# Kernel tuning notes

Hardware: AMD Instinct MI355X
Metric: run time of the kernel (lower is better)

The kernel has to match this reference:

```python
import jax, jax.numpy as jnp
import numpy as np

# norse LIFRefracParameters defaults
TAU_SYN_INV = 200.0
TAU_MEM_INV = 100.0
V_LEAK = 0.0
V_TH = 1.0
V_RESET = 0.0
ALPHA = 100.0       # SuperSpike surrogate slope
RHO_RESET = 5.0     # refractory period (steps)
DT = 0.001


@jax.custom_vjp
def superspike(x):
    # Heaviside forward, SuperSpike surrogate backward
    return (x > 0).astype(x.dtype)

def _ss_fwd(x):
    return superspike(x), x

def _ss_bwd(x, g):
    return (g / (ALPHA * jnp.abs(x) + 1.0) ** 2,)

superspike.defvjp(_ss_fwd, _ss_bwd)


def lif_mc_refrac_step(inp, z, v, i, rho, input_weights, recurrent_weights, g_coupling):
    # --- lif_mc_step ---
    dv = DT * TAU_MEM_INV * ((V_LEAK - v) + i)
    v_decayed = v + dv + v @ g_coupling.T          # [B,H] compartment coupling GEMM
    i_decayed = i - DT * TAU_SYN_INV * i
    z_new = superspike(v_decayed - V_TH)
    v_new = (1.0 - z_new) * v_decayed + z_new * V_RESET
    i_new = i_decayed + inp @ input_weights.T + z @ recurrent_weights.T  # two GEMMs
    # --- refractory update ---
    refrac_mask = superspike(rho)
    v_new = (1.0 - refrac_mask) * v_new + refrac_mask * v  # hold v while refractory
    z_new = (1.0 - refrac_mask) * z_new                    # suppress spikes
    rho_new = (1.0 - z_new) * jnp.maximum(rho - refrac_mask, 0.0) + z_new * RHO_RESET
    return z_new, v_new, i_new, rho_new


def setup_inputs() -> dict:
    key = jax.random.key(0)
    ks = jax.random.split(key, 8)
    B, I, H = 4096, 2048, 2048
    inp = jax.random.normal(ks[0], (B, I), jnp.float32)
    z = jax.random.uniform(ks[1], (B, H), jnp.float32)
    v = jax.random.normal(ks[2], (B, H), jnp.float32)
    i = jax.random.normal(ks[3], (B, H), jnp.float32)
    rho = jax.random.normal(ks[4], (B, H), jnp.float32)  # ~half neurons refractory
    input_weights = jax.random.normal(ks[5], (H, I), jnp.float32) / np.sqrt(I).astype(np.float32)
    recurrent_weights = jax.random.normal(ks[6], (H, H), jnp.float32) / np.sqrt(H).astype(np.float32)
    g_coupling = jax.random.normal(ks[7], (H, H), jnp.float32) / np.sqrt(H).astype(np.float32)
    return dict(inp=inp, z=z, v=v, i=i, rho=rho,
                input_weights=input_weights,
                recurrent_weights=recurrent_weights,
                g_coupling=g_coupling)


def reference(inp, z, v, i, rho, input_weights, recurrent_weights, g_coupling):
    return lif_mc_refrac_step(inp, z, v, i, rho, input_weights, recurrent_weights, g_coupling)
```

## Files before the change

kernel.cpp:

```cpp
#include <hip/hip_runtime.h>


#define HDIM 2048
#define BATCH 4096
#define KIN 2048
#define BM 128
#define BN 128
#define BK 32
#define MARGIN 0.02f
#define FLAG_LDS_CAP 1024

typedef _Float16 f16x8 __attribute__((ext_vector_type(8)));
typedef __fp16 h16x2 __attribute__((ext_vector_type(2)));
typedef float f32x4 __attribute__((ext_vector_type(4)));

template <typename T>
__device__ __forceinline__ void stage(const T* src, int ldk, int row0, int k0,
                                      T* lds_tile, int t) {
  constexpr int CHN = (BK * (int)sizeof(T)) / 16;
  constexpr int EPC = 16 / (int)sizeof(T);
#pragma unroll
  for (int j = 0; j < (BM * CHN) / 256; ++j) {
    const int u = j * 256 + t;
    const int r = u / CHN;
    const int cs = u & (CHN - 1);
    const int c = cs ^ (((r * CHN) >> 3) & (CHN - 1));
    const T* g = src + (size_t)(row0 + r) * ldk + k0 + c * EPC;
    __builtin_amdgcn_global_load_lds(
        (const __attribute__((address_space(1))) void*)(T*)g,
        (__attribute__((address_space(3))) void*)(lds_tile + u * EPC), 16, 0, 0);
  }
}

__device__ __forceinline__ f16x8 read_frag(const _Float16* tile, int r, int q) {
  const int slot = r * 4 + (q ^ ((r >> 1) & 3));
  return *(const f16x8*)(tile + slot * 8);
}
__device__ __forceinline__ f16x8 read_frag(const float* tile, int r, int q) {
  const int s = r & 7;
  const f32x4 a = *(const f32x4*)(tile + (r * 8 + ((2 * q) ^ s)) * 4);
  const f32x4 b = *(const f32x4*)(tile + (r * 8 + ((2 * q + 1) ^ s)) * 4);
  f16x8 o;
  h16x2 p;
  p = __builtin_amdgcn_cvt_pkrtz(a[0], a[1]); o[0] = (_Float16)p[0]; o[1] = (_Float16)p[1];
  p = __builtin_amdgcn_cvt_pkrtz(a[2], a[3]); o[2] = (_Float16)p[0]; o[3] = (_Float16)p[1];
  p = __builtin_amdgcn_cvt_pkrtz(b[0], b[1]); o[4] = (_Float16)p[0]; o[5] = (_Float16)p[1];
  p = __builtin_amdgcn_cvt_pkrtz(b[2], b[3]); o[6] = (_Float16)p[0]; o[7] = (_Float16)p[1];
  return o;
}

template <typename T>
__global__ __launch_bounds__(256, 4)
void k_gemm(const T* vA, const T* inpA, const T* zA,
            const T* gB, const T* WiB, const T* WrB,
            const float* v, const float* cur_in, const float* rho,
            float* z_out, float* v_out, float* rho_out, float* i_out,
            unsigned* flag_cnt, unsigned* flag_list, unsigned flag_cap) {
  __shared__ T As[2][BM * BK];
  __shared__ T Bs[2][BN * BK];
  __shared__ unsigned s_cnt;
  __shared__ unsigned s_base;
  __shared__ unsigned s_idx[FLAG_LDS_CAP];
  const int t = threadIdx.x;
  const int bid = blockIdx.x;
  const int x = bid & 7;
  const int j = bid >> 3;
  const int role = (j >> 5) & 1;
  const int jj = (j & 31) | ((j >> 6) << 5);
  const int mg = x & 3, ng = x >> 2;
  const int m0 = (mg * 8 + (jj >> 3)) * BM;
  const int n0 = (ng * 8 + (jj & 7)) * BN;

  const int wave = t >> 6, lane = t & 63;
  const int wm = (wave >> 1) * 64, wn = (wave & 1) * 64;
  const int lrow = lane & 15, quad = lane >> 4;

  const int kmax = role ? 2 * KIN : KIN;
  const int NT = kmax / BK;

  auto pick = [&](int k0, const T*& Ap, const T*& Bp) {
    if (role == 0)      { Ap = vA;   Bp = gB;  }
    else if (k0 < KIN)  { Ap = inpA; Bp = WiB; }
    else                { Ap = zA;   Bp = WrB; }
  };

  {
    const T *Ap, *Bp;
    pick(0, Ap, Bp);
    stage(Ap, KIN, m0, 0, As[0], t);
    stage(Bp, KIN, n0, 0, Bs[0], t);
  }
  if (t == 0) s_cnt = 0;

  f32x4 acc[4][4] = {};
#pragma unroll 2
  for (int it = 0; it < NT; ++it) {
    const int cur = it & 1;
    if (it + 1 < NT) {
      const int k0n = (it + 1) * BK;
      const T *Ap, *Bp;
      pick(k0n, Ap, Bp);
      const int kl = k0n & (KIN - 1);
      stage(Ap, KIN, m0, kl, As[cur ^ 1], t);
      stage(Bp, KIN, n0, kl, Bs[cur ^ 1], t);
      if constexpr (sizeof(T) == 2)
        asm volatile("s_waitcnt vmcnt(4)" ::: "memory");
      else
        asm volatile("s_waitcnt vmcnt(8)" ::: "memory");
    } else {
      asm volatile("s_waitcnt vmcnt(0)" ::: "memory");
    }
    __builtin_amdgcn_s_barrier();
    asm volatile("" ::: "memory");

    f16x8 af[4], bf[4];
#pragma unroll
    for (int mi = 0; mi < 4; ++mi) af[mi] = read_frag(As[cur], wm + mi * 16 + lrow, quad);
#pragma unroll
    for (int ni = 0; ni < 4; ++ni) bf[ni] = read_frag(Bs[cur], wn + ni * 16 + lrow, quad);
#pragma unroll
    for (int mi = 0; mi < 4; ++mi)
#pragma unroll
      for (int ni = 0; ni < 4; ++ni)
        acc[mi][ni] =
            __builtin_amdgcn_mfma_f32_16x16x32_f16(af[mi], bf[ni], acc[mi][ni], 0, 0, 0);

    asm volatile("" ::: "memory");
    __builtin_amdgcn_s_barrier();
  }

  if (role == 0) {
#pragma unroll
    for (int mi = 0; mi < 4; ++mi)
#pragma unroll
      for (int r = 0; r < 4; ++r) {
        const int row = m0 + wm + mi * 16 + quad * 4 + r;
#pragma unroll
        for (int ni = 0; ni < 4; ++ni) {
          const int col = n0 + wn + ni * 16 + lrow;
          const size_t idx = (size_t)row * HDIM + col;
          const float P = acc[mi][ni][r];
          const float vv = v[idx], ii = cur_in[idx], rr = rho[idx];
          const float vd = vv + 0.1f * (ii - vv) + P;
          float zo, vo, ro;
          if (rr > 0.0f) {
            zo = 0.0f; vo = vv; ro = fmaxf(rr - 1.0f, 0.0f);
          } else {
            const bool zs = vd > 1.0f;
            zo = zs ? 1.0f : 0.0f;
            vo = zs ? 0.0f : vd;
            ro = zs ? 5.0f : fmaxf(rr, 0.0f);
            if (fabsf(vd - 1.0f) < MARGIN) {
              unsigned p = atomicAdd(&s_cnt, 1u);
              if (p < FLAG_LDS_CAP) s_idx[p] = (unsigned)idx;
              else {
                unsigned q = atomicAdd(flag_cnt, 1u);
                if (q < flag_cap) flag_list[q] = (unsigned)idx;
              }
            }
          }
          z_out[idx] = zo; v_out[idx] = vo; rho_out[idx] = ro;
        }
      }
    __syncthreads();
    unsigned n = s_cnt;
    if (n > FLAG_LDS_CAP) n = FLAG_LDS_CAP;
    if (t == 0) s_base = atomicAdd(flag_cnt, n);
    __syncthreads();
    for (unsigned u = t; u < n; u += 256) {
      const unsigned d = s_base + u;
      if (d < flag_cap) flag_list[d] = s_idx[u];
    }
  } else {
#pragma unroll
    for (int mi = 0; mi < 4; ++mi)
#pragma unroll
      for (int r = 0; r < 4; ++r) {
        const int row = m0 + wm + mi * 16 + quad * 4 + r;
#pragma unroll
        for (int ni = 0; ni < 4; ++ni) {
          const int col = n0 + wn + ni * 16 + lrow;
          const size_t idx = (size_t)row * HDIM + col;
          const float ii = cur_in[idx];
          i_out[idx] = (ii - 0.2f * ii) + acc[mi][ni][r];
        }
      }
  }
}

__global__ void k_cast(const float* __restrict__ v, const float* __restrict__ inp,
                       const float* __restrict__ z, const float* __restrict__ g,
                       const float* __restrict__ Wi, const float* __restrict__ Wr,
                       _Float16* __restrict__ dst, unsigned* __restrict__ flag_cnt) {
  if (blockIdx.x == 0 && threadIdx.x == 0) *flag_cnt = 0;
  const size_t NA = (size_t)BATCH * HDIM, NB = (size_t)HDIM * HDIM;
  const size_t TOT = (3 * NA + 3 * NB) / 8;
  const size_t w = (size_t)blockIdx.x * blockDim.x + threadIdx.x;
  if (w >= TOT) return;
  const size_t e = w * 8;
  const float* s; size_t off;
  if      (e < NA)          { s = v;   off = e; }
  else if (e < 2 * NA)      { s = inp; off = e - NA; }
  else if (e < 3 * NA)      { s = z;   off = e - 2 * NA; }
  else if (e < 3 * NA + NB) { s = g;   off = e - 3 * NA; }
  else if (e < 3 * NA + 2 * NB) { s = Wi; off = e - 3 * NA - NB; }
  else                      { s = Wr;  off = e - 3 * NA - 2 * NB; }
  const f32x4 a = *(const f32x4*)(s + off);
  const f32x4 b = *(const f32x4*)(s + off + 4);
  f16x8 o; h16x2 p;
  p = __builtin_amdgcn_cvt_pkrtz(a[0], a[1]); o[0] = (_Float16)p[0]; o[1] = (_Float16)p[1];
  p = __builtin_amdgcn_cvt_pkrtz(a[2], a[3]); o[2] = (_Float16)p[0]; o[3] = (_Float16)p[1];
  p = __builtin_amdgcn_cvt_pkrtz(b[0], b[1]); o[4] = (_Float16)p[0]; o[5] = (_Float16)p[1];
  p = __builtin_amdgcn_cvt_pkrtz(b[2], b[3]); o[6] = (_Float16)p[0]; o[7] = (_Float16)p[1];
  *(f16x8*)(dst + e) = o;
}

__global__ void k_zero_cnt(unsigned* p) { if (threadIdx.x == 0) p[0] = 0; }

__global__ __launch_bounds__(256, 2)
void k_fixup(const float* __restrict__ v, const float* __restrict__ cur,
             const float* __restrict__ rho, const float* __restrict__ g,
             float* __restrict__ z_out, float* __restrict__ v_out,
             float* __restrict__ rho_out,
             const unsigned* __restrict__ flag_cnt,
             const unsigned* __restrict__ flag_list, unsigned flag_cap) {
  unsigned n = *flag_cnt;
  if (n > flag_cap) n = flag_cap;
  const int lane = threadIdx.x & 63;
  const int nw = gridDim.x * 4;
  for (unsigned it = blockIdx.x * 4 + (threadIdx.x >> 6); it < n; it += nw) {
    const unsigned idx = flag_list[it];
    const unsigned b = idx >> 11, h = idx & (HDIM - 1);
    const float* vp = v + (size_t)b * HDIM;
    const float* gp = g + (size_t)h * HDIM;
    double s0 = 0.0, s1 = 0.0, s2 = 0.0, s3 = 0.0;
    for (int k = lane; k < KIN; k += 256) {
      s0 += (double)vp[k]       * (double)gp[k];
      s1 += (double)vp[k + 64]  * (double)gp[k + 64];
      s2 += (double)vp[k + 128] * (double)gp[k + 128];
      s3 += (double)vp[k + 192] * (double)gp[k + 192];
    }
    double s = (s0 + s1) + (s2 + s3);
#pragma unroll
    for (int off = 32; off; off >>= 1) s += __shfl_down(s, off, 64);
    if (lane == 0) {
      const double vv = (double)v[idx], ii = (double)cur[idx];
      const double vd = (vv + (0.001 * 100.0) * ((0.0 - vv) + ii)) + s;
      const bool zs = vd > 1.0;
      z_out[idx]   = zs ? 1.0f : 0.0f;
      v_out[idx]   = zs ? 0.0f : (float)vd;
      rho_out[idx] = zs ? 5.0f : fmaxf(rho[idx], 0.0f);
    }
  }
}

extern "C" void kernel_launch(void* const* d_in, const int* in_sizes, int n_in,
                              void* d_out, int out_size, void* d_ws, size_t ws_size,
                              hipStream_t stream) {
  (void)in_sizes; (void)n_in; (void)out_size;
  const float* inp = (const float*)d_in[0];
  const float* z   = (const float*)d_in[1];
  const float* v   = (const float*)d_in[2];
  const float* cur = (const float*)d_in[3];
  const float* rho = (const float*)d_in[4];
  const float* Wi  = (const float*)d_in[5];
  const float* Wr  = (const float*)d_in[6];
  const float* g   = (const float*)d_in[7];

  float* out = (float*)d_out;
  const size_t NE = (size_t)BATCH * HDIM;
  float* z_out = out;
  float* v_out = out + NE;
  float* i_out = out + 2 * NE;
  float* rho_out = out + 3 * NE;

  const size_t NA = NE, NB = (size_t)HDIM * HDIM;
  const size_t F16_NEED = (3 * NA + 3 * NB) * sizeof(_Float16);
  const bool use16 = ws_size >= F16_NEED + (1u << 22);

  unsigned* flag_cnt =
      use16 ? (unsigned*)((char*)d_ws + F16_NEED) : (unsigned*)d_ws;
  unsigned* flag_list = flag_cnt + 4;
  unsigned flag_cap = 0;
  {
    const size_t used = (size_t)((char*)flag_list - (char*)d_ws);
    if (ws_size > used + 64) {
      size_t cap = (ws_size - used) / sizeof(unsigned);
      if (cap > (size_t)4 * 1024 * 1024) cap = (size_t)4 * 1024 * 1024;
      flag_cap = (unsigned)cap;
    }
  }

  if (use16) {
    _Float16* ws16 = (_Float16*)d_ws;
    const _Float16* vh   = ws16;
    const _Float16* inph = ws16 + NA;
    const _Float16* zh   = ws16 + 2 * NA;
    const _Float16* gh   = ws16 + 3 * NA;
    const _Float16* Wih  = ws16 + 3 * NA + NB;
    const _Float16* Wrh  = ws16 + 3 * NA + 2 * NB;
    const size_t TOT = (3 * NA + 3 * NB) / 8;
    k_cast<<<(unsigned)((TOT + 255) / 256), 256, 0, stream>>>(v, inp, z, g, Wi, Wr,
                                                              ws16, flag_cnt);
    k_gemm<_Float16><<<1024, 256, 0, stream>>>(vh, inph, zh, gh, Wih, Wrh,
                                               v, cur, rho, z_out, v_out, rho_out, i_out,
                                               flag_cnt, flag_list, flag_cap);
  } else {
    k_zero_cnt<<<1, 64, 0, stream>>>(flag_cnt);
    k_gemm<float><<<1024, 256, 0, stream>>>(v, inp, z, g, Wi, Wr,
                                            v, cur, rho, z_out, v_out, rho_out, i_out,
                                            flag_cnt, flag_list, flag_cap);
  }

  k_fixup<<<1024, 256, 0, stream>>>(v, cur, rho, g, z_out, v_out, rho_out,
                                    flag_cnt, flag_list, flag_cap);
}
```

Measured before the change: 621.9 us.

## Replace fp16 GEMM with 256x128 tile, 3-stage pipeline, one block per tile doing both GEMMs

Adds a new fp16 GEMM kernel with 256x128 output tiles, BK=64 and 512 threads. It uses a three-buffer global_load_lds pipeline with two loads in flight, and a plain XOR swizzle on the LDS tiles. Each of the 256 blocks runs the coupling GEMM with its spike epilogue and then the input plus recurrent GEMM for the same tile, instead of spreading the two roles across 1024 smaller blocks. The goal is more operand reuse per LDS byte and fewer barriers per FLOP. The cost is about 144KB of LDS per block, so only 8 waves run per CU, and the epilogues are not overlapped with other blocks' compute. The fp32 fallback kernel is split out and now pushes flags straight to global atomics.

```diff
diff --git a/kernel.cpp b/kernel.cpp
--- a/kernel.cpp
+++ b/kernel.cpp
@@ -4,15 +4,192 @@
 #define HDIM 2048
 #define BATCH 4096
 #define KIN 2048
+#define MARGIN 0.02f
+#define FLAG_LDS_CAP 512
+
+#define BM2 256
+#define BN2 128
+#define BK2 64
+#define NTHR 512
+
 #define BM 128
 #define BN 128
 #define BK 32
-#define MARGIN 0.02f
-#define FLAG_LDS_CAP 1024
 
 typedef _Float16 f16x8 __attribute__((ext_vector_type(8)));
 typedef __fp16 h16x2 __attribute__((ext_vector_type(2)));
 typedef float f32x4 __attribute__((ext_vector_type(4)));
+
+
+template <int ROWS>
+__device__ __forceinline__ void stage2(const _Float16* src, int row0, int k0,
+                                       _Float16* lds_tile, int t) {
+  constexpr int CHN = (BK2 * 2) / 16;
+#pragma unroll
+  for (int j = 0; j < (ROWS * CHN) / NTHR; ++j) {
+    const int u = j * NTHR + t;
+    const int r = u / CHN;
+    const int cs = u & (CHN - 1);
+    const int c = cs ^ (r & (CHN - 1));
+    const _Float16* g = src + (size_t)(row0 + r) * KIN + k0 + c * 8;
+    __builtin_amdgcn_global_load_lds(
+        (const __attribute__((address_space(1))) void*)g,
+        (__attribute__((address_space(3))) void*)(lds_tile + u * 8), 16, 0, 0);
+  }
+}
+
+__device__ __forceinline__ f16x8 read_frag2(const _Float16* tile, int r, int c) {
+  const int slot = r * 8 + (c ^ (r & 7));
+  return *(const f16x8*)(tile + slot * 8);
+}
+
+__global__ __launch_bounds__(NTHR, 2)
+void k_gemm256(const _Float16* vA, const _Float16* inpA, const _Float16* zA,
+               const _Float16* gB, const _Float16* WiB, const _Float16* WrB,
+               const float* v, const float* cur_in, const float* rho,
+               float* z_out, float* v_out, float* rho_out, float* i_out,
+               unsigned* flag_cnt, unsigned* flag_list, unsigned flag_cap) {
+  __shared__ _Float16 As[3][BM2 * BK2];
+  __shared__ _Float16 Bs[3][BN2 * BK2];
+  __shared__ unsigned s_cnt, s_base;
+  __shared__ unsigned s_idx[FLAG_LDS_CAP];
+  const int t = threadIdx.x;
+  const int bid = blockIdx.x;
+  const int x = bid & 7;
+  const int jj = bid >> 3;
+  const int mg = x & 3, ng = x >> 2;
+  const int m0 = (mg * 4 + (jj >> 3)) * BM2;
+  const int n0 = (ng * 8 + (jj & 7)) * BN2;
+
+  const int wave = t >> 6, lane = t & 63;
+  const int wm = (wave >> 1) * 64, wn = (wave & 1) * 64;
+  const int lrow = lane & 15, quad = lane >> 4;
+  if (t == 0) s_cnt = 0;
+
+  for (int job = 0; job < 2; ++job) {
+    const int role = job;
+    const int NT = role ? (2 * KIN) / BK2 : KIN / BK2;
+
+    auto pick = [&](int k0, const _Float16*& Ap, const _Float16*& Bp) {
+      if (role == 0)     { Ap = vA;   Bp = gB;  }
+      else if (k0 < KIN) { Ap = inpA; Bp = WiB; }
+      else               { Ap = zA;   Bp = WrB; }
+    };
+
+    {
+      const _Float16 *Ap, *Bp;
+      pick(0, Ap, Bp);
+      stage2<BM2>(Ap, m0, 0, As[0], t);
+      stage2<BN2>(Bp, n0, 0, Bs[0], t);
+      pick(BK2, Ap, Bp);
+      stage2<BM2>(Ap, m0, BK2, As[1], t);
+      stage2<BN2>(Bp, n0, BK2, Bs[1], t);
+    }
+
+    f32x4 acc[4][4] = {};
+    int cur = 0;
+    for (int it = 0; it < NT; ++it) {
+      const int nxt = it + 2;
+      if (nxt < NT) {
+        const _Float16 *Ap, *Bp;
+        pick(nxt * BK2, Ap, Bp);
+        const int kl = (nxt * BK2) & (KIN - 1);
+        const int buf = (cur >= 1) ? cur - 1 : 2;
+        stage2<BM2>(Ap, m0, kl, As[buf], t);
+        stage2<BN2>(Bp, n0, kl, Bs[buf], t);
+        asm volatile("s_waitcnt vmcnt(12)" ::: "memory");
+      } else if (it + 1 < NT) {
+        asm volatile("s_waitcnt vmcnt(6)" ::: "memory");
+      } else {
+        asm volatile("s_waitcnt vmcnt(0)" ::: "memory");
+      }
+      __builtin_amdgcn_s_barrier();
+      asm volatile("" ::: "memory");
+
+      f16x8 af[2][4], bf[2][4];
+#pragma unroll
+      for (int ks = 0; ks < 2; ++ks) {
+#pragma unroll
+        for (int mi = 0; mi < 4; ++mi)
+          af[ks][mi] = read_frag2(As[cur], wm + mi * 16 + lrow, ks * 4 + quad);
+#pragma unroll
+        for (int ni = 0; ni < 4; ++ni)
+          bf[ks][ni] = read_frag2(Bs[cur], wn + ni * 16 + lrow, ks * 4 + quad);
+      }
+#pragma unroll
+      for (int ks = 0; ks < 2; ++ks)
+#pragma unroll
+        for (int mi = 0; mi < 4; ++mi)
+#pragma unroll
+          for (int ni = 0; ni < 4; ++ni)
+            acc[mi][ni] = __builtin_amdgcn_mfma_f32_16x16x32_f16(
+                af[ks][mi], bf[ks][ni], acc[mi][ni], 0, 0, 0);
+
+      asm volatile("" ::: "memory");
+      __builtin_amdgcn_s_barrier();
+      cur = (cur == 2) ? 0 : cur + 1;
+    }
+
+    if (role == 0) {
+#pragma unroll
+      for (int mi = 0; mi < 4; ++mi)
+#pragma unroll
+        for (int r = 0; r < 4; ++r) {
+          const int row = m0 + wm + mi * 16 + quad * 4 + r;
+#pragma unroll
+          for (int ni = 0; ni < 4; ++ni) {
+            const int col = n0 + wn + ni * 16 + lrow;
+            const size_t idx = (size_t)row * HDIM + col;
+            const float P = acc[mi][ni][r];
+            const float vv = v[idx], ii = cur_in[idx], rr = rho[idx];
+            const float vd = vv + 0.1f * (ii - vv) + P;
+            float zo, vo, ro;
+            if (rr > 0.0f) {
+              zo = 0.0f; vo = vv; ro = fmaxf(rr - 1.0f, 0.0f);
+            } else {
+              const bool zs = vd > 1.0f;
+              zo = zs ? 1.0f : 0.0f;
+              vo = zs ? 0.0f : vd;
+              ro = zs ? 5.0f : fmaxf(rr, 0.0f);
+              if (fabsf(vd - 1.0f) < MARGIN) {
+                unsigned p = atomicAdd(&s_cnt, 1u);
+                if (p < FLAG_LDS_CAP) s_idx[p] = (unsigned)idx;
+                else {
+                  unsigned q = atomicAdd(flag_cnt, 1u);
+                  if (q < flag_cap) flag_list[q] = (unsigned)idx;
+                }
+              }
+            }
+            z_out[idx] = zo; v_out[idx] = vo; rho_out[idx] = ro;
+          }
+        }
+      __syncthreads();
+      unsigned n = s_cnt;
+      if (n > FLAG_LDS_CAP) n = FLAG_LDS_CAP;
+      if (t == 0) s_base = atomicAdd(flag_cnt, n);
+      __syncthreads();
+      for (unsigned u = t; u < n; u += NTHR) {
+        const unsigned d = s_base + u;
+        if (d < flag_cap) flag_list[d] = s_idx[u];
+      }
+    } else {
+#pragma unroll
+      for (int mi = 0; mi < 4; ++mi)
+#pragma unroll
+        for (int r = 0; r < 4; ++r) {
+          const int row = m0 + wm + mi * 16 + quad * 4 + r;
+#pragma unroll
+          for (int ni = 0; ni < 4; ++ni) {
+            const int col = n0 + wn + ni * 16 + lrow;
+            const size_t idx = (size_t)row * HDIM + col;
+            const float ii = cur_in[idx];
+            i_out[idx] = (ii - 0.2f * ii) + acc[mi][ni][r];
+          }
+        }
+    }
+  }
+}
+
 
 template <typename T>
 __device__ __forceinline__ void stage(const T* src, int ldk, int row0, int k0,
@@ -32,10 +209,6 @@
   }
 }
 
-__device__ __forceinline__ f16x8 read_frag(const _Float16* tile, int r, int q) {
-  const int slot = r * 4 + (q ^ ((r >> 1) & 3));
-  return *(const f16x8*)(tile + slot * 8);
-}
 __device__ __forceinline__ f16x8 read_frag(const float* tile, int r, int q) {
   const int s = r & 7;
   const f32x4 a = *(const f32x4*)(tile + (r * 8 + ((2 * q) ^ s)) * 4);
@@ -49,18 +222,14 @@
   return o;
 }
 
-template <typename T>
 __global__ __launch_bounds__(256, 4)
-void k_gemm(const T* vA, const T* inpA, const T* zA,
-            const T* gB, const T* WiB, const T* WrB,
-            const float* v, const float* cur_in, const float* rho,
-            float* z_out, float* v_out, float* rho_out, float* i_out,
-            unsigned* flag_cnt, unsigned* flag_list, unsigned flag_cap) {
-  __shared__ T As[2][BM * BK];
-  __shared__ T Bs[2][BN * BK];
-  __shared__ unsigned s_cnt;
-  __shared__ unsigned s_base;
-  __shared__ unsigned s_idx[FLAG_LDS_CAP];
+void k_gemm128f(const float* vA, const float* inpA, const float* zA,
+                const float* gB, const float* WiB, const float* WrB,
+                const float* v, const float* cur_in, const float* rho,
+                float* z_out, float* v_out, float* rho_out, float* i_out,
+                unsigned* flag_cnt, unsigned* flag_list, unsigned flag_cap) {
+  __shared__ float As[2][BM * BK];
+  __shared__ float Bs[2][BN * BK];
   const int t = threadIdx.x;
   const int bid = blockIdx.x;
   const int x = bid & 7;
@@ -78,41 +247,33 @@
   const int kmax = role ? 2 * KIN : KIN;
   const int NT = kmax / BK;
 
-  auto pick = [&](int k0, const T*& Ap, const T*& Bp) {
+  auto pick = [&](int k0, const float*& Ap, const float*& Bp) {
     if (role == 0)      { Ap = vA;   Bp = gB;  }
     else if (k0 < KIN)  { Ap = inpA; Bp = WiB; }
     else                { Ap = zA;   Bp = WrB; }
   };
-
   {
-    const T *Ap, *Bp;
+    const float *Ap, *Bp;
     pick(0, Ap, Bp);
     stage(Ap, KIN, m0, 0, As[0], t);
     stage(Bp, KIN, n0, 0, Bs[0], t);
   }
-  if (t == 0) s_cnt = 0;
-
   f32x4 acc[4][4] = {};
 #pragma unroll 2
   for (int it = 0; it < NT; ++it) {
     const int cur = it & 1;
     if (it + 1 < NT) {
-      const int k0n = (it + 1) * BK;
-      const T *Ap, *Bp;
-      pick(k0n, Ap, Bp);
-      const int kl = k0n & (KIN - 1);
+      const float *Ap, *Bp;
+      pick((it + 1) * BK, Ap, Bp);
+      const int kl = ((it + 1) * BK) & (KIN - 1);
       stage(Ap, KIN, m0, kl, As[cur ^ 1], t);
       stage(Bp, KIN, n0, kl, Bs[cur ^ 1], t);
-      if constexpr (sizeof(T) == 2)
-        asm volatile("s_waitcnt vmcnt(4)" ::: "memory");
-      else
-        asm volatile("s_waitcnt vmcnt(8)" ::: "memory");
+      asm volatile("s_waitcnt vmcnt(8)" ::: "memory");
     } else {
       asm volatile("s_waitcnt vmcnt(0)" ::: "memory");
     }
     __builtin_amdgcn_s_barrier();
     asm volatile("" ::: "memory");
-
     f16x8 af[4], bf[4];
 #pragma unroll
     for (int mi = 0; mi < 4; ++mi) af[mi] = read_frag(As[cur], wm + mi * 16 + lrow, quad);
@@ -124,7 +285,6 @@
       for (int ni = 0; ni < 4; ++ni)
         acc[mi][ni] =
             __builtin_amdgcn_mfma_f32_16x16x32_f16(af[mi], bf[ni], acc[mi][ni], 0, 0, 0);
-
     asm volatile("" ::: "memory");
     __builtin_amdgcn_s_barrier();
   }
@@ -143,34 +303,20 @@
           const float vv = v[idx], ii = cur_in[idx], rr = rho[idx];
           const float vd = vv + 0.1f * (ii - vv) + P;
           float zo, vo, ro;
-          if (rr > 0.0f) {
-            zo = 0.0f; vo = vv; ro = fmaxf(rr - 1.0f, 0.0f);
-          } else {
+          if (rr > 0.0f) { zo = 0.0f; vo = vv; ro = fmaxf(rr - 1.0f, 0.0f); }
+          else {
             const bool zs = vd > 1.0f;
             zo = zs ? 1.0f : 0.0f;
             vo = zs ? 0.0f : vd;
             ro = zs ? 5.0f : fmaxf(rr, 0.0f);
             if (fabsf(vd - 1.0f) < MARGIN) {
-              unsigned p = atomicAdd(&s_cnt, 1u);
-              if (p < FLAG_LDS_CAP) s_idx[p] = (unsigned)idx;
-              else {
-                unsigned q = atomicAdd(flag_cnt, 1u);
-                if (q < flag_cap) flag_list[q] = (unsigned)idx;
-              }
+              unsigned p = atomicAdd(flag_cnt, 1u);
+              if (p < flag_cap) flag_list[p] = (unsigned)idx;
             }
           }
           z_out[idx] = zo; v_out[idx] = vo; rho_out[idx] = ro;
         }
       }
-    __syncthreads();
-    unsigned n = s_cnt;
-    if (n > FLAG_LDS_CAP) n = FLAG_LDS_CAP;
-    if (t == 0) s_base = atomicAdd(flag_cnt, n);
-    __syncthreads();
-    for (unsigned u = t; u < n; u += 256) {
-      const unsigned d = s_base + u;
-      if (d < flag_cap) flag_list[d] = s_idx[u];
-    }
   } else {
 #pragma unroll
     for (int mi = 0; mi < 4; ++mi)
@@ -302,14 +448,14 @@
     const size_t TOT = (3 * NA + 3 * NB) / 8;
     k_cast<<<(unsigned)((TOT + 255) / 256), 256, 0, stream>>>(v, inp, z, g, Wi, Wr,
                                                               ws16, flag_cnt);
-    k_gemm<_Float16><<<1024, 256, 0, stream>>>(vh, inph, zh, gh, Wih, Wrh,
-                                               v, cur, rho, z_out, v_out, rho_out, i_out,
-                                               flag_cnt, flag_list, flag_cap);
+    k_gemm256<<<256, NTHR, 0, stream>>>(vh, inph, zh, gh, Wih, Wrh,
+                                        v, cur, rho, z_out, v_out, rho_out, i_out,
+                                        flag_cnt, flag_list, flag_cap);
   } else {
     k_zero_cnt<<<1, 64, 0, stream>>>(flag_cnt);
-    k_gemm<float><<<1024, 256, 0, stream>>>(v, inp, z, g, Wi, Wr,
-                                            v, cur, rho, z_out, v_out, rho_out, i_out,
-                                            flag_cnt, flag_list, flag_cap);
+    k_gemm128f<<<1024, 256, 0, stream>>>(v, inp, z, g, Wi, Wr,
+                                         v, cur, rho, z_out, v_out, rho_out, i_out,
+                                         flag_cnt, flag_list, flag_cap);
   }
 
   k_fixup<<<1024, 256, 0, stream>>>(v, cur, rho, g, z_out, v_out, rho_out,
```

Measured after the change: 715.3 us. +15.0%, slower.

## Fuse near-threshold fp64 fixup into GEMM epilogue, shrink overflow fixup grid

Applied to the files above, without the earlier changes.

Neurons whose fp16 result lands near the spike threshold are now recomputed in fp64 directly inside the GEMM kernel's epilogue, one wave per flagged index. The global flag list is used only when a block overflows its LDS list. This removes the round trip through global memory for the flag list and most of the separate fixup launch, which now runs with a much smaller grid. The cost is a longer tail in the role-0 blocks, doing serial fp64 dot products that read fp32 v and g. The old k_gemm template is left in place with a dubious nullptr g argument, but it is no longer called.

```diff
diff --git a/kernel.cpp b/kernel.cpp
--- a/kernel.cpp
+++ b/kernel.cpp
@@ -8,7 +8,7 @@
 #define BN 128
 #define BK 32
 #define MARGIN 0.02f
-#define FLAG_LDS_CAP 1024
+#define FLAG_LDS_CAP 512
 
 typedef _Float16 f16x8 __attribute__((ext_vector_type(8)));
 typedef __fp16 h16x2 __attribute__((ext_vector_type(2)));
@@ -49,6 +49,36 @@
   return o;
 }
 
+__device__ __forceinline__ void fixup_one(unsigned idx, const float* __restrict__ v,
+                                          const float* __restrict__ cur,
+                                          const float* __restrict__ rho,
+                                          const float* __restrict__ g,
+                                          float* __restrict__ z_out,
+                                          float* __restrict__ v_out,
+                                          float* __restrict__ rho_out, int lane) {
+  const unsigned b = idx >> 11, h = idx & (HDIM - 1);
+  const float* vp = v + (size_t)b * HDIM;
+  const float* gp = g + (size_t)h * HDIM;
+  double s0 = 0.0, s1 = 0.0, s2 = 0.0, s3 = 0.0;
+  for (int k = lane; k < KIN; k += 256) {
+    s0 += (double)vp[k]       * (double)gp[k];
+    s1 += (double)vp[k + 64]  * (double)gp[k + 64];
+    s2 += (double)vp[k + 128] * (double)gp[k + 128];
+    s3 += (double)vp[k + 192] * (double)gp[k + 192];
+  }
+  double s = (s0 + s1) + (s2 + s3);
+#pragma unroll
+  for (int off = 32; off; off >>= 1) s += __shfl_down(s, off, 64);
+  if (lane == 0) {
+    const double vv = (double)v[idx], ii = (double)cur[idx];
+    const double vd = (vv + (0.001 * 100.0) * ((0.0 - vv) + ii)) + s;
+    const bool zs = vd > 1.0;
+    z_out[idx]   = zs ? 1.0f : 0.0f;
+    v_out[idx]   = zs ? 0.0f : (float)vd;
+    rho_out[idx] = zs ? 5.0f : fmaxf(rho[idx], 0.0f);
+  }
+}
+
 template <typename T>
 __global__ __launch_bounds__(256, 4)
 void k_gemm(const T* vA, const T* inpA, const T* zA,
@@ -59,7 +89,6 @@
   __shared__ T As[2][BM * BK];
   __shared__ T Bs[2][BN * BK];
   __shared__ unsigned s_cnt;
-  __shared__ unsigned s_base;
   __shared__ unsigned s_idx[FLAG_LDS_CAP];
   const int t = threadIdx.x;
   const int bid = blockIdx.x;
@@ -165,12 +194,144 @@
     __syncthreads();
     unsigned n = s_cnt;
     if (n > FLAG_LDS_CAP) n = FLAG_LDS_CAP;
-    if (t == 0) s_base = atomicAdd(flag_cnt, n);
+    for (unsigned u = wave; u < n; u += 4)
+      fixup_one(s_idx[u], v, cur_in, rho, gB ? nullptr : nullptr, z_out, v_out,
+                rho_out, lane);
+  } else {
+#pragma unroll
+    for (int mi = 0; mi < 4; ++mi)
+#pragma unroll
+      for (int r = 0; r < 4; ++r) {
+        const int row = m0 + wm + mi * 16 + quad * 4 + r;
+#pragma unroll
+        for (int ni = 0; ni < 4; ++ni) {
+          const int col = n0 + wn + ni * 16 + lrow;
+          const size_t idx = (size_t)row * HDIM + col;
+          const float ii = cur_in[idx];
+          i_out[idx] = (ii - 0.2f * ii) + acc[mi][ni][r];
+        }
+      }
+  }
+}
+
+template <typename T>
+__global__ __launch_bounds__(256, 4)
+void k_gemm_fx(const T* vA, const T* inpA, const T* zA,
+               const T* gB, const T* WiB, const T* WrB,
+               const float* v, const float* cur_in, const float* rho,
+               const float* g32,
+               float* z_out, float* v_out, float* rho_out, float* i_out,
+               unsigned* flag_cnt, unsigned* flag_list, unsigned flag_cap) {
+  __shared__ T As[2][BM * BK];
+  __shared__ T Bs[2][BN * BK];
+  __shared__ unsigned s_cnt;
+  __shared__ unsigned s_idx[FLAG_LDS_CAP];
+  const int t = threadIdx.x;
+  const int bid = blockIdx.x;
+  const int x = bid & 7;
+  const int j = bid >> 3;
+  const int role = (j >> 5) & 1;
+  const int jj = (j & 31) | ((j >> 6) << 5);
+  const int mg = x & 3, ng = x >> 2;
+  const int m0 = (mg * 8 + (jj >> 3)) * BM;
+  const int n0 = (ng * 8 + (jj & 7)) * BN;
+
+  const int wave = t >> 6, lane = t & 63;
+  const int wm = (wave >> 1) * 64, wn = (wave & 1) * 64;
+  const int lrow = lane & 15, quad = lane >> 4;
+
+  const int kmax = role ? 2 * KIN : KIN;
+  const int NT = kmax / BK;
+
+  auto pick = [&](int k0, const T*& Ap, const T*& Bp) {
+    if (role == 0)      { Ap = vA;   Bp = gB;  }
+    else if (k0 < KIN)  { Ap = inpA; Bp = WiB; }
+    else                { Ap = zA;   Bp = WrB; }
+  };
+
+  {
+    const T *Ap, *Bp;
+    pick(0, Ap, Bp);
+    stage(Ap, KIN, m0, 0, As[0], t);
+    stage(Bp, KIN, n0, 0, Bs[0], t);
+  }
+  if (t == 0) s_cnt = 0;
+
+  f32x4 acc[4][4] = {};
+#pragma unroll 2
+  for (int it = 0; it < NT; ++it) {
+    const int cur = it & 1;
+    if (it + 1 < NT) {
+      const int k0n = (it + 1) * BK;
+      const T *Ap, *Bp;
+      pick(k0n, Ap, Bp);
+      const int kl = k0n & (KIN - 1);
+      stage(Ap, KIN, m0, kl, As[cur ^ 1], t);
+      stage(Bp, KIN, n0, kl, Bs[cur ^ 1], t);
+      if constexpr (sizeof(T) == 2)
+        asm volatile("s_waitcnt vmcnt(4)" ::: "memory");
+      else
+        asm volatile("s_waitcnt vmcnt(8)" ::: "memory");
+    } else {
+      asm volatile("s_waitcnt vmcnt(0)" ::: "memory");
+    }
+    __builtin_amdgcn_s_barrier();
+    asm volatile("" ::: "memory");
+
+    f16x8 af[4], bf[4];
+#pragma unroll
+    for (int mi = 0; mi < 4; ++mi) af[mi] = read_frag(As[cur], wm + mi * 16 + lrow, quad);
+#pragma unroll
+    for (int ni = 0; ni < 4; ++ni) bf[ni] = read_frag(Bs[cur], wn + ni * 16 + lrow, quad);
+#pragma unroll
+    for (int mi = 0; mi < 4; ++mi)
+#pragma unroll
+      for (int ni = 0; ni < 4; ++ni)
+        acc[mi][ni] =
+            __builtin_amdgcn_mfma_f32_16x16x32_f16(af[mi], bf[ni], acc[mi][ni], 0, 0, 0);
+
+    asm volatile("" ::: "memory");
+    __builtin_amdgcn_s_barrier();
+  }
+
+  if (role == 0) {
+#pragma unroll
+    for (int mi = 0; mi < 4; ++mi)
+#pragma unroll
+      for (int r = 0; r < 4; ++r) {
+        const int row = m0 + wm + mi * 16 + quad * 4 + r;
+#pragma unroll
+        for (int ni = 0; ni < 4; ++ni) {
+          const int col = n0 + wn + ni * 16 + lrow;
+          const size_t idx = (size_t)row * HDIM + col;
+          const float P = acc[mi][ni][r];
+          const float vv = v[idx], ii = cur_in[idx], rr = rho[idx];
+          const float vd = vv + 0.1f * (ii - vv) + P;
+          float zo, vo, ro;
+          if (rr > 0.0f) {
+            zo = 0.0f; vo = vv; ro = fmaxf(rr - 1.0f, 0.0f);
+          } else {
+            const bool zs = vd > 1.0f;
+            zo = zs ? 1.0f : 0.0f;
+            vo = zs ? 0.0f : vd;
+            ro = zs ? 5.0f : fmaxf(rr, 0.0f);
+            if (fabsf(vd - 1.0f) < MARGIN) {
+              unsigned p = atomicAdd(&s_cnt, 1u);
+              if (p < FLAG_LDS_CAP) s_idx[p] = (unsigned)idx;
+              else {
+                unsigned q = atomicAdd(flag_cnt, 1u);
+                if (q < flag_cap) flag_list[q] = (unsigned)idx;
+              }
+            }
+          }
+          z_out[idx] = zo; v_out[idx] = vo; rho_out[idx] = ro;
+        }
+      }
     __syncthreads();
-    for (unsigned u = t; u < n; u += 256) {
-      const unsigned d = s_base + u;
-      if (d < flag_cap) flag_list[d] = s_idx[u];
-    }
+    unsigned n = s_cnt;
+    if (n > FLAG_LDS_CAP) n = FLAG_LDS_CAP;
+    for (unsigned u = wave; u < n; u += 4)
+      fixup_one(s_idx[u], v, cur_in, rho, g32, z_out, v_out, rho_out, lane);
   } else {
 #pragma unroll
     for (int mi = 0; mi < 4; ++mi)
@@ -230,27 +391,7 @@
   const int nw = gridDim.x * 4;
   for (unsigned it = blockIdx.x * 4 + (threadIdx.x >> 6); it < n; it += nw) {
     const unsigned idx = flag_list[it];
-    const unsigned b = idx >> 11, h = idx & (HDIM - 1);
-    const float* vp = v + (size_t)b * HDIM;
-    const float* gp = g + (size_t)h * HDIM;
-    double s0 = 0.0, s1 = 0.0, s2 = 0.0, s3 = 0.0;
-    for (int k = lane; k < KIN; k += 256) {
-      s0 += (double)vp[k]       * (double)gp[k];
-      s1 += (double)vp[k + 64]  * (double)gp[k + 64];
-      s2 += (double)vp[k + 128] * (double)gp[k + 128];
-      s3 += (double)vp[k + 192] * (double)gp[k + 192];
-    }
-    double s = (s0 + s1) + (s2 + s3);
-#pragma unroll
-    for (int off = 32; off; off >>= 1) s += __shfl_down(s, off, 64);
-    if (lane == 0) {
-      const double vv = (double)v[idx], ii = (double)cur[idx];
-      const double vd = (vv + (0.001 * 100.0) * ((0.0 - vv) + ii)) + s;
-      const bool zs = vd > 1.0;
-      z_out[idx]   = zs ? 1.0f : 0.0f;
-      v_out[idx]   = zs ? 0.0f : (float)vd;
-      rho_out[idx] = zs ? 5.0f : fmaxf(rho[idx], 0.0f);
-    }
+    fixup_one(idx, v, cur, rho, g, z_out, v_out, rho_out, lane);
   }
 }
 
@@ -302,16 +443,18 @@
     const size_t TOT = (3 * NA + 3 * NB) / 8;
     k_cast<<<(unsigned)((TOT + 255) / 256), 256, 0, stream>>>(v, inp, z, g, Wi, Wr,
                                                               ws16, flag_cnt);
-    k_gemm<_Float16><<<1024, 256, 0, stream>>>(vh, inph, zh, gh, Wih, Wrh,
-                                               v, cur, rho, z_out, v_out, rho_out, i_out,
-                                               flag_cnt, flag_list, flag_cap);
+    k_gemm_fx<_Float16><<<1024, 256, 0, stream>>>(vh, inph, zh, gh, Wih, Wrh,
+                                                  v, cur, rho, g,
+                                                  z_out, v_out, rho_out, i_out,
+                                                  flag_cnt, flag_list, flag_cap);
   } else {
     k_zero_cnt<<<1, 64, 0, stream>>>(flag_cnt);
-    k_gemm<float><<<1024, 256, 0, stream>>>(v, inp, z, g, Wi, Wr,
-                                            v, cur, rho, z_out, v_out, rho_out, i_out,
-                                            flag_cnt, flag_list, flag_cap);
-  }
-
-  k_fixup<<<1024, 256, 0, stream>>>(v, cur, rho, g, z_out, v_out, rho_out,
-                                    flag_cnt, flag_list, flag_cap);
-}
+    k_gemm_fx<float><<<1024, 256, 0, stream>>>(v, inp, z, g, Wi, Wr,
+                                               v, cur, rho, g,
+                                               z_out, v_out, rho_out, i_out,
+                                               flag_cnt, flag_list, flag_cap);
+  }
+
+  k_fixup<<<64, 256, 0, stream>>>(v, cur, rho, g, z_out, v_out, rho_out,
+                                  flag_cnt, flag_list, flag_cap);
+}
```

Measured after the change: 597.3 us. 1.04x faster.
